# Kernel tuning notes

Hardware: AMD Instinct MI355X
Metric: run time of the kernel (lower is better)

## Reference

```python
import jax, jax.numpy as jnp
import numpy as np

NUM_FEATURE = 128  # bins; linear in_features = NUM_FEATURE + 1
VECTOR_DIM = 64


def setup_inputs() -> dict:
    key = jax.random.key(0)
    k1, k2, k3 = jax.random.split(key, 3)
    x = jax.random.randint(k1, (8192, 200), 0, NUM_FEATURE + 1)
    # nn.Linear(num_feature+1, vector_dim): W is (out, in) = (64, 129)
    W = jax.random.normal(k2, (VECTOR_DIM, NUM_FEATURE + 1), dtype=jnp.float32) * 0.05
    b = jax.random.normal(k3, (VECTOR_DIM,), dtype=jnp.float32) * 0.05
    return {"x": x, "W": W, "b": b}


def reference(x, W, b):
    # embeddings = tril(ones)[x] has ones in columns 0..x (inclusive), so
    # embeddings @ W.T = sum_{j<=x} W[:, j] = cumsum(W, axis=1)[:, x].
    # This avoids materializing the (..., F+1) one-hot-prefix tensor.
    Wc = jnp.cumsum(W, axis=1)              # (D, F+1)
    out = jnp.take(Wc.T, x, axis=0) + b     # (8192, 200, D)
    return out
```

## Files before the change

### kernel.cpp

```cpp
#include <hip/hip_runtime.h>


constexpr int F1   = 129;
constexpr int D    = 64;
constexpr int ROWS = 8192 * 200;
constexpr int TBL_F = F1 * D;
constexpr int TBL4  = TBL_F / 4;

constexpr int BLOCKS = 1024;
constexpr int TPB    = 512;
constexpr int ROWS_PER_BLOCK = ROWS / BLOCKS;
constexpr int Q_PER_BLOCK    = ROWS_PER_BLOCK * D / 4;
constexpr int ITERS          = Q_PER_BLOCK / TPB;

typedef float floatx4 __attribute__((ext_vector_type(4)));

__global__ __launch_bounds__(256) void build_table_kernel(
        const float* __restrict__ W,
        const float* __restrict__ b,
        float* __restrict__ tbl) {
    __shared__ float ldsW[TBL_F];
    for (int i = threadIdx.x; i < TBL_F; i += 256)
        ldsW[i] = W[i];
    __syncthreads();
    int d = threadIdx.x;
    if (d < D) {
        float acc = b[d];
        for (int j = 0; j < F1; ++j) {
            acc += ldsW[d * F1 + j];
            tbl[j * D + d] = acc;
        }
    }
}

__global__ __launch_bounds__(TPB, 8) void embed_main_kernel(
        const int* __restrict__ x,
        const float* __restrict__ tbl,
        float* __restrict__ out) {
    __shared__ floatx4 lds_tbl[TBL4];
    __shared__ int     lds_x[ROWS_PER_BLOCK];

    const floatx4* t4 = (const floatx4*)tbl;
    for (int i = threadIdx.x; i < TBL4; i += TPB)
        lds_tbl[i] = t4[i];
    const int row0 = blockIdx.x * ROWS_PER_BLOCK;
    for (int i = threadIdx.x; i < ROWS_PER_BLOCK; i += TPB)
        lds_x[i] = x[row0 + i];
    __syncthreads();

    floatx4* out4 = (floatx4*)out + (size_t)blockIdx.x * Q_PER_BLOCK;
#pragma unroll 5
    for (int it = 0; it < ITERS; ++it) {
        int j    = it * TPB + threadIdx.x;
        int xi   = lds_x[j >> 4];
        floatx4 v = lds_tbl[xi * 16 + (j & 15)];
        out4[j] = v;
    }
}

extern "C" void kernel_launch(void* const* d_in, const int* in_sizes, int n_in,
                              void* d_out, int out_size, void* d_ws, size_t ws_size,
                              hipStream_t stream) {
    const int*   x = (const int*)  d_in[0];
    const float* W = (const float*)d_in[1];
    const float* b = (const float*)d_in[2];
    float* out = (float*)d_out;
    float* tbl = (float*)d_ws;

    build_table_kernel<<<1, 256, 0, stream>>>(W, b, tbl);
    embed_main_kernel<<<BLOCKS, TPB, 0, stream>>>(x, tbl, out);
}
```

Before: 422.0 us.

## Drop LDS staging and gather table rows directly from global memory with grid-stride

Removes the per-block copy of the cumulative table and index slice into LDS and the barrier, and instead reads x and the table directly from global memory (relying on cache) in a grid-stride loop over all output quads. Block count and size change to 2048x256 with unroll 8. This drops the redundant per-block table load (33KB per block) and raises occupancy by freeing LDS, but each thread now makes an uncached-in-LDS gather per output, and 16 lanes reread the same x entry.

After: 442.9 us. 1.05x slower.

```diff
diff --git a/kernel.cpp b/kernel.cpp
--- a/kernel.cpp
+++ b/kernel.cpp
@@ -4,14 +4,13 @@
 constexpr int F1   = 129;
 constexpr int D    = 64;
 constexpr int ROWS = 8192 * 200;
-constexpr int TBL_F = F1 * D;
-constexpr int TBL4  = TBL_F / 4;
+constexpr int TOTAL4 = ROWS * D / 4;
+constexpr int TBL_F  = F1 * D;
 
-constexpr int BLOCKS = 1024;
-constexpr int TPB    = 512;
-constexpr int ROWS_PER_BLOCK = ROWS / BLOCKS;
-constexpr int Q_PER_BLOCK    = ROWS_PER_BLOCK * D / 4;
-constexpr int ITERS          = Q_PER_BLOCK / TPB;
+constexpr int BLOCKS = 2048;
+constexpr int TPB    = 256;
+constexpr int THREADS = BLOCKS * TPB;
+constexpr int ITERS   = TOTAL4 / THREADS;
 
 typedef float floatx4 __attribute__((ext_vector_type(4)));
 
@@ -33,28 +32,21 @@
     }
 }
 
-__global__ __launch_bounds__(TPB, 8) void embed_main_kernel(
+__global__ __launch_bounds__(TPB) void embed_main_kernel(
         const int* __restrict__ x,
         const float* __restrict__ tbl,
         float* __restrict__ out) {
-    __shared__ floatx4 lds_tbl[TBL4];
-    __shared__ int     lds_x[ROWS_PER_BLOCK];
-
     const floatx4* t4 = (const floatx4*)tbl;
-    for (int i = threadIdx.x; i < TBL4; i += TPB)
-        lds_tbl[i] = t4[i];
-    const int row0 = blockIdx.x * ROWS_PER_BLOCK;
-    for (int i = threadIdx.x; i < ROWS_PER_BLOCK; i += TPB)
-        lds_x[i] = x[row0 + i];
-    __syncthreads();
-
-    floatx4* out4 = (floatx4*)out + (size_t)blockIdx.x * Q_PER_BLOCK;
-#pragma unroll 5
+    floatx4* out4 = (floatx4*)out;
+    const int base = blockIdx.x * TPB + threadIdx.x;
+#pragma unroll 8
     for (int it = 0; it < ITERS; ++it) {
-        int j    = it * TPB + threadIdx.x;
-        int xi   = lds_x[j >> 4];
-        floatx4 v = lds_tbl[xi * 16 + (j & 15)];
-        out4[j] = v;
+        int idx  = it * THREADS + base;
+        int row  = idx >> 4;
+        int quad = idx & 15;
+        int xi   = x[row];
+        floatx4 v = t4[xi * 16 + quad];
+        out4[idx] = v;
     }
 }
 
```
